# Kernel tuning notes

Measured on AMD Instinct MI355X. Metric: run time of the kernel, lower is better.

The kernel has to match this reference:

```python
import jax, jax.numpy as jnp
import numpy as np

B, T, I, H, O = 256, 512, 128, 256, 1


def setup_inputs() -> dict:
    key = jax.random.key(0)
    ks = jax.random.split(key, 7)
    s_ih = 1.0 / np.sqrt(H)
    return {
        "x": jax.random.normal(ks[0], (B, T, I), dtype=jnp.float32),
        "W_ih": jax.random.uniform(ks[1], (H, I), jnp.float32, -s_ih, s_ih),
        "W_hh": jax.random.uniform(ks[2], (H, H), jnp.float32, -s_ih, s_ih),
        "b_ih": jax.random.uniform(ks[3], (H,), jnp.float32, -s_ih, s_ih),
        "b_hh": jax.random.uniform(ks[4], (H,), jnp.float32, -s_ih, s_ih),
        "fc_w": jax.random.uniform(ks[5], (O, H), jnp.float32, -s_ih, s_ih),
        "fc_b": jax.random.uniform(ks[6], (O,), jnp.float32, -s_ih, s_ih),
    }


def reference(x, W_ih, W_hh, b_ih, b_hh, fc_w, fc_b):
    # Elman RNN (tanh), batch_first, single layer, h0 = zeros.
    # Only the last hidden state feeds the fc head, so scan carries h only.
    b = b_ih + b_hh
    xW = jnp.einsum('bti,hi->tbh', x, W_ih) + b  # precompute input projection [T,B,H]

    def step(h, xw_t):
        h = jnp.tanh(xw_t + h @ W_hh.T)
        return h, None

    h0 = jnp.zeros((x.shape[0], W_hh.shape[0]), dtype=x.dtype)
    h_last, _ = jax.lax.scan(step, h0, xW)
    return h_last @ fc_w.T + fc_b  # [B, O]
```

## Files before the change

### kernel.cpp

```cpp
#include <hip/hip_runtime.h>
#include <hip/hip_bf16.h>

#define B_ 256
#define T_ 512
#define I_ 128
#define H_ 256

#define SC 2.885390081777927f

typedef __bf16 bf16x8 __attribute__((ext_vector_type(8)));
typedef float  f32x4  __attribute__((ext_vector_type(4)));
typedef unsigned short u16;
typedef unsigned int   u32;

union U16x8Cast { uint4 v; bf16x8 b; };

__device__ inline u16 f2b(float f) {
    union { __bf16 h; u16 u; } c; c.h = (__bf16)f; return c.u;
}
__device__ inline bf16x8 pack8(float4 lo, float4 hi) {
    bf16x8 f;
    f[0]=(__bf16)lo.x; f[1]=(__bf16)lo.y; f[2]=(__bf16)lo.z; f[3]=(__bf16)lo.w;
    f[4]=(__bf16)hi.x; f[5]=(__bf16)hi.y; f[6]=(__bf16)hi.z; f[7]=(__bf16)hi.w;
    return f;
}
__device__ inline bf16x8 pack8s(float4 lo, float4 hi, float s) {
    bf16x8 f;
    f[0]=(__bf16)(lo.x*s); f[1]=(__bf16)(lo.y*s); f[2]=(__bf16)(lo.z*s); f[3]=(__bf16)(lo.w*s);
    f[4]=(__bf16)(hi.x*s); f[5]=(__bf16)(hi.y*s); f[6]=(__bf16)(hi.z*s); f[7]=(__bf16)(hi.w*s);
    return f;
}
__device__ inline uint2 pack4(float a, float b, float c, float d) {
    uint2 p;
    p.x = (u32)f2b(a) | ((u32)f2b(b) << 16);
    p.y = (u32)f2b(c) | ((u32)f2b(d) << 16);
    return p;
}
__device__ inline f32x4 b4_to_f32x4(uint2 u) {
    f32x4 r;
    r[0] = __uint_as_float(u.x << 16);
    r[1] = __uint_as_float(u.x & 0xFFFF0000u);
    r[2] = __uint_as_float(u.y << 16);
    r[3] = __uint_as_float(u.y & 0xFFFF0000u);
    return r;
}
__device__ inline float tanh_pre(float s) {
    float e = __builtin_amdgcn_exp2f(s);
    float r = __builtin_amdgcn_rcpf(1.f + e);
    return fmaf(-2.f, r, 1.f);
}

#define WG_BARRIER() asm volatile("s_waitcnt lgkmcnt(0)\n\ts_barrier" ::: "memory")

#define LDST 264
__global__ __launch_bounds__(256, 2) void xw_gemm_mfma(const float* __restrict__ x,
                                                       const float* __restrict__ W_ih,
                                                       const float* __restrict__ b_ih,
                                                       const float* __restrict__ b_hh,
                                                       u16* __restrict__ xw) {
    __shared__ u16 tile[64 * LDST];

    const int tid  = (int)threadIdx.x;
    const int wave = tid >> 6;
    const int lane = tid & 63;
    const int q    = lane >> 4;
    const int ml   = lane & 15;
    const int m0   = (int)blockIdx.x * 64;
    const int b    = m0 >> 9;
    const int t0   = m0 & 511;
    const int n0   = wave * 64;

    bf16x8 wA[4][4];
#pragma unroll
    for (int tau = 0; tau < 4; ++tau) {
        const float* wr = W_ih + (size_t)(n0 + tau * 16 + ml) * I_;
#pragma unroll
        for (int kap = 0; kap < 4; ++kap) {
            const int k0 = kap * 32 + q * 8;
            wA[tau][kap] = pack8s(*(const float4*)(wr + k0), *(const float4*)(wr + k0 + 4), SC);
        }
    }

    f32x4 acc[4][4];
#pragma unroll
    for (int mt = 0; mt < 4; ++mt)
#pragma unroll
        for (int tau = 0; tau < 4; ++tau) acc[mt][tau] = (f32x4)0.f;

#pragma unroll
    for (int kap = 0; kap < 4; ++kap) {
        bf16x8 xB[4];
#pragma unroll
        for (int mt = 0; mt < 4; ++mt) {
            const float* xr = x + (size_t)(m0 + mt * 16 + ml) * I_ + kap * 32 + q * 8;
            xB[mt] = pack8(*(const float4*)xr, *(const float4*)(xr + 4));
        }
#pragma unroll
        for (int mt = 0; mt < 4; ++mt)
#pragma unroll
            for (int tau = 0; tau < 4; ++tau)
                acc[mt][tau] = __builtin_amdgcn_mfma_f32_16x16x32_bf16(
                    wA[tau][kap], xB[mt], acc[mt][tau], 0, 0, 0);
    }

    float4 bias4[4];
#pragma unroll
    for (int tau = 0; tau < 4; ++tau) {
        const int n = n0 + tau * 16 + q * 4;
        float4 bi = *(const float4*)(b_ih + n);
        float4 bh = *(const float4*)(b_hh + n);
        bias4[tau] = make_float4((bi.x + bh.x) * SC, (bi.y + bh.y) * SC,
                                 (bi.z + bh.z) * SC, (bi.w + bh.w) * SC);
    }

#pragma unroll
    for (int mt = 0; mt < 4; ++mt) {
        const int row = mt * 16 + ml;
#pragma unroll
        for (int tau = 0; tau < 4; ++tau) {
            uint2 pk = pack4(acc[mt][tau][0] + bias4[tau].x,
                             acc[mt][tau][1] + bias4[tau].y,
                             acc[mt][tau][2] + bias4[tau].z,
                             acc[mt][tau][3] + bias4[tau].w);
            *(uint2*)(tile + row * LDST + n0 + tau * 16 + q * 4) = pk;
        }
    }
    __syncthreads();
#pragma unroll
    for (int s = 0; s < 4; ++s) {
        const int rr = s * 16 + (tid >> 4);
        const int c  = tid & 15;
        const uint4* srcp = (const uint4*)(tile + rr * LDST);
        uint4* dstp = (uint4*)(xw + ((size_t)(t0 + rr) * B_ + b) * H_);
        uint4 v0 = srcp[c];
        uint4 v1 = srcp[c + 16];
        dstp[c] = v0;
        dstp[c + 16] = v1;
    }
}

__global__ __launch_bounds__(512, 2) void rnn_scan_mfma(const u16* __restrict__ xw,
                                                        const float* __restrict__ W_hh,
                                                        const float* __restrict__ fc_w,
                                                        const float* __restrict__ fc_b,
                                                        float* __restrict__ out) {
    __shared__ __attribute__((aligned(16))) u16 hbuf[2][4096];
    __shared__ float red[8][16];

    const int tid  = (int)threadIdx.x;
    const int wave = tid >> 6;
    const int lane = tid & 63;
    const int q    = lane >> 4;
    const int m    = lane & 15;
    const int b0   = (int)blockIdx.x * 16;

    bf16x8 wf[2][8];
#pragma unroll
    for (int tau2 = 0; tau2 < 2; ++tau2) {
        const float* wr = W_hh + (size_t)(wave * 32 + tau2 * 16 + m) * H_;
#pragma unroll
        for (int kap = 0; kap < 8; ++kap) {
            const int k0 = kap * 32 + q * 8;
            wf[tau2][kap] = pack8s(*(const float4*)(wr + k0), *(const float4*)(wr + k0 + 4), SC);
        }
    }

    int widx[2];
#pragma unroll
    for (int tau2 = 0; tau2 < 2; ++tau2) {
        const int nbw = wave * 32 + tau2 * 16 + q * 4;
        widx[tau2] = (nbw >> 5) * 512 + (((nbw >> 3) & 3) * 16 + m) * 8 + (nbw & 7);
    }

    {
        uint4* p = (uint4*)&hbuf[0][0];
        const uint4 z = {0u, 0u, 0u, 0u};
        p[tid] = z;
    }
    WG_BARRIER();

    const u16* xwp = xw + (size_t)(b0 + m) * H_ + (wave * 32 + q * 4);
    const size_t tstride = (size_t)B_ * H_;

    uint2 pfA[2], pfB[2];
    pfA[0] = *(const uint2*)(xwp);
    pfA[1] = *(const uint2*)(xwp + 16);
    pfB[0] = *(const uint2*)(xwp + tstride);
    pfB[1] = *(const uint2*)(xwp + tstride + 16);

    int cur = 0;
    f32x4 acc[2];
    for (int tt = 0; tt < T_ / 2; ++tt) {
        {
            const int t = 2 * tt;
            acc[0] = b4_to_f32x4(pfA[0]);
            acc[1] = b4_to_f32x4(pfA[1]);
            if (t + 2 < T_) {
                const u16* pt = xwp + (size_t)(t + 2) * tstride;
                pfA[0] = *(const uint2*)(pt);
                pfA[1] = *(const uint2*)(pt + 16);
            }
            const uint4* hb = (const uint4*)&hbuf[cur][0];
#pragma unroll
            for (int kap = 0; kap < 8; ++kap) {
                U16x8Cast c; c.v = hb[kap * 64 + lane];
                acc[0] = __builtin_amdgcn_mfma_f32_16x16x32_bf16(wf[0][kap], c.b, acc[0], 0, 0, 0);
                acc[1] = __builtin_amdgcn_mfma_f32_16x16x32_bf16(wf[1][kap], c.b, acc[1], 0, 0, 0);
            }
            u16* wb = &hbuf[cur ^ 1][0];
#pragma unroll
            for (int tau2 = 0; tau2 < 2; ++tau2) {
                uint2 pk = pack4(tanh_pre(acc[tau2][0]), tanh_pre(acc[tau2][1]),
                                 tanh_pre(acc[tau2][2]), tanh_pre(acc[tau2][3]));
                *(uint2*)(wb + widx[tau2]) = pk;
            }
            WG_BARRIER();
            cur ^= 1;
        }
        {
            const int t = 2 * tt + 1;
            acc[0] = b4_to_f32x4(pfB[0]);
            acc[1] = b4_to_f32x4(pfB[1]);
            if (t + 2 < T_) {
                const u16* pt = xwp + (size_t)(t + 2) * tstride;
                pfB[0] = *(const uint2*)(pt);
                pfB[1] = *(const uint2*)(pt + 16);
            }
            const uint4* hb = (const uint4*)&hbuf[cur][0];
#pragma unroll
            for (int kap = 0; kap < 8; ++kap) {
                U16x8Cast c; c.v = hb[kap * 64 + lane];
                acc[0] = __builtin_amdgcn_mfma_f32_16x16x32_bf16(wf[0][kap], c.b, acc[0], 0, 0, 0);
                acc[1] = __builtin_amdgcn_mfma_f32_16x16x32_bf16(wf[1][kap], c.b, acc[1], 0, 0, 0);
            }
            if (t != T_ - 1) {
                u16* wb = &hbuf[cur ^ 1][0];
#pragma unroll
                for (int tau2 = 0; tau2 < 2; ++tau2) {
                    uint2 pk = pack4(tanh_pre(acc[tau2][0]), tanh_pre(acc[tau2][1]),
                                     tanh_pre(acc[tau2][2]), tanh_pre(acc[tau2][3]));
                    *(uint2*)(wb + widx[tau2]) = pk;
                }
                WG_BARRIER();
                cur ^= 1;
            }
        }
    }

    float4 fcw[2];
#pragma unroll
    for (int tau2 = 0; tau2 < 2; ++tau2)
        fcw[tau2] = *(const float4*)(fc_w + wave * 32 + tau2 * 16 + q * 4);

    float partial = 0.f;
#pragma unroll
    for (int tau2 = 0; tau2 < 2; ++tau2) {
        partial += tanh_pre(acc[tau2][0]) * fcw[tau2].x;
        partial += tanh_pre(acc[tau2][1]) * fcw[tau2].y;
        partial += tanh_pre(acc[tau2][2]) * fcw[tau2].z;
        partial += tanh_pre(acc[tau2][3]) * fcw[tau2].w;
    }
    partial += __shfl_xor(partial, 16);
    partial += __shfl_xor(partial, 32);
    __syncthreads();
    if (lane < 16) red[wave][m] = partial;
    __syncthreads();
    if (tid < 16) {
        float s = red[0][tid] + red[1][tid] + red[2][tid] + red[3][tid]
                + red[4][tid] + red[5][tid] + red[6][tid] + red[7][tid];
        out[b0 + tid] = s + fc_b[0];
    }
}

extern "C" void kernel_launch(void* const* d_in, const int* in_sizes, int n_in,
                              void* d_out, int out_size, void* d_ws, size_t ws_size,
                              hipStream_t stream) {
    const float* x    = (const float*)d_in[0];
    const float* W_ih = (const float*)d_in[1];
    const float* W_hh = (const float*)d_in[2];
    const float* b_ih = (const float*)d_in[3];
    const float* b_hh = (const float*)d_in[4];
    const float* fc_w = (const float*)d_in[5];
    const float* fc_b = (const float*)d_in[6];
    float* out = (float*)d_out;

    u16* xwbuf = (u16*)d_ws;
    xw_gemm_mfma<<<(B_ * T_) / 64, 256, 0, stream>>>(x, W_ih, b_ih, b_hh, xwbuf);
    rnn_scan_mfma<<<B_ / 16, 512, 0, stream>>>(xwbuf, W_hh, fc_w, fc_b, out);
}
```

Measured before the change: 387.1 us.

## Fuse input projection into recurrent scan kernel, dropping separate GEMM and workspace

Removes the separate xW GEMM kernel and its bf16 workspace round-trip. Each scan step now loads the raw x row for the next timestep and computes the input projection with extra MFMAs inside the recurrence, using W_ih fragments held in registers. This saves a kernel launch and the memory traffic for the intermediate, but it adds 8 MFMAs per step to the serial critical path, and only 16 blocks run, so HBM reads of x per step may add latency.

```diff
diff --git a/kernel.cpp b/kernel.cpp
--- a/kernel.cpp
+++ b/kernel.cpp
@@ -36,14 +36,6 @@
     p.y = (u32)f2b(c) | ((u32)f2b(d) << 16);
     return p;
 }
-__device__ inline f32x4 b4_to_f32x4(uint2 u) {
-    f32x4 r;
-    r[0] = __uint_as_float(u.x << 16);
-    r[1] = __uint_as_float(u.x & 0xFFFF0000u);
-    r[2] = __uint_as_float(u.y << 16);
-    r[3] = __uint_as_float(u.y & 0xFFFF0000u);
-    return r;
-}
 __device__ inline float tanh_pre(float s) {
     float e = __builtin_amdgcn_exp2f(s);
     float r = __builtin_amdgcn_rcpf(1.f + e);
@@ -52,98 +44,14 @@
 
 #define WG_BARRIER() asm volatile("s_waitcnt lgkmcnt(0)\n\ts_barrier" ::: "memory")
 
-#define LDST 264
-__global__ __launch_bounds__(256, 2) void xw_gemm_mfma(const float* __restrict__ x,
-                                                       const float* __restrict__ W_ih,
-                                                       const float* __restrict__ b_ih,
-                                                       const float* __restrict__ b_hh,
-                                                       u16* __restrict__ xw) {
-    __shared__ u16 tile[64 * LDST];
-
-    const int tid  = (int)threadIdx.x;
-    const int wave = tid >> 6;
-    const int lane = tid & 63;
-    const int q    = lane >> 4;
-    const int ml   = lane & 15;
-    const int m0   = (int)blockIdx.x * 64;
-    const int b    = m0 >> 9;
-    const int t0   = m0 & 511;
-    const int n0   = wave * 64;
-
-    bf16x8 wA[4][4];
-#pragma unroll
-    for (int tau = 0; tau < 4; ++tau) {
-        const float* wr = W_ih + (size_t)(n0 + tau * 16 + ml) * I_;
-#pragma unroll
-        for (int kap = 0; kap < 4; ++kap) {
-            const int k0 = kap * 32 + q * 8;
-            wA[tau][kap] = pack8s(*(const float4*)(wr + k0), *(const float4*)(wr + k0 + 4), SC);
-        }
-    }
-
-    f32x4 acc[4][4];
-#pragma unroll
-    for (int mt = 0; mt < 4; ++mt)
-#pragma unroll
-        for (int tau = 0; tau < 4; ++tau) acc[mt][tau] = (f32x4)0.f;
-
-#pragma unroll
-    for (int kap = 0; kap < 4; ++kap) {
-        bf16x8 xB[4];
-#pragma unroll
-        for (int mt = 0; mt < 4; ++mt) {
-            const float* xr = x + (size_t)(m0 + mt * 16 + ml) * I_ + kap * 32 + q * 8;
-            xB[mt] = pack8(*(const float4*)xr, *(const float4*)(xr + 4));
-        }
-#pragma unroll
-        for (int mt = 0; mt < 4; ++mt)
-#pragma unroll
-            for (int tau = 0; tau < 4; ++tau)
-                acc[mt][tau] = __builtin_amdgcn_mfma_f32_16x16x32_bf16(
-                    wA[tau][kap], xB[mt], acc[mt][tau], 0, 0, 0);
-    }
-
-    float4 bias4[4];
-#pragma unroll
-    for (int tau = 0; tau < 4; ++tau) {
-        const int n = n0 + tau * 16 + q * 4;
-        float4 bi = *(const float4*)(b_ih + n);
-        float4 bh = *(const float4*)(b_hh + n);
-        bias4[tau] = make_float4((bi.x + bh.x) * SC, (bi.y + bh.y) * SC,
-                                 (bi.z + bh.z) * SC, (bi.w + bh.w) * SC);
-    }
-
-#pragma unroll
-    for (int mt = 0; mt < 4; ++mt) {
-        const int row = mt * 16 + ml;
-#pragma unroll
-        for (int tau = 0; tau < 4; ++tau) {
-            uint2 pk = pack4(acc[mt][tau][0] + bias4[tau].x,
-                             acc[mt][tau][1] + bias4[tau].y,
-                             acc[mt][tau][2] + bias4[tau].z,
-                             acc[mt][tau][3] + bias4[tau].w);
-            *(uint2*)(tile + row * LDST + n0 + tau * 16 + q * 4) = pk;
-        }
-    }
-    __syncthreads();
-#pragma unroll
-    for (int s = 0; s < 4; ++s) {
-        const int rr = s * 16 + (tid >> 4);
-        const int c  = tid & 15;
-        const uint4* srcp = (const uint4*)(tile + rr * LDST);
-        uint4* dstp = (uint4*)(xw + ((size_t)(t0 + rr) * B_ + b) * H_);
-        uint4 v0 = srcp[c];
-        uint4 v1 = srcp[c + 16];
-        dstp[c] = v0;
-        dstp[c + 16] = v1;
-    }
-}
-
-__global__ __launch_bounds__(512, 2) void rnn_scan_mfma(const u16* __restrict__ xw,
-                                                        const float* __restrict__ W_hh,
-                                                        const float* __restrict__ fc_w,
-                                                        const float* __restrict__ fc_b,
-                                                        float* __restrict__ out) {
+__global__ __launch_bounds__(512, 1) void rnn_fused(const float* __restrict__ x,
+                                                    const float* __restrict__ W_ih,
+                                                    const float* __restrict__ W_hh,
+                                                    const float* __restrict__ b_ih,
+                                                    const float* __restrict__ b_hh,
+                                                    const float* __restrict__ fc_w,
+                                                    const float* __restrict__ fc_b,
+                                                    float* __restrict__ out) {
     __shared__ __attribute__((aligned(16))) u16 hbuf[2][4096];
     __shared__ float red[8][16];
 
@@ -164,6 +72,28 @@
             wf[tau2][kap] = pack8s(*(const float4*)(wr + k0), *(const float4*)(wr + k0 + 4), SC);
         }
     }
+    bf16x8 wi[2][4];
+#pragma unroll
+    for (int tau2 = 0; tau2 < 2; ++tau2) {
+        const float* wr = W_ih + (size_t)(wave * 32 + tau2 * 16 + m) * I_;
+#pragma unroll
+        for (int kap = 0; kap < 4; ++kap) {
+            const int k0 = kap * 32 + q * 8;
+            wi[tau2][kap] = pack8s(*(const float4*)(wr + k0), *(const float4*)(wr + k0 + 4), SC);
+        }
+    }
+
+    f32x4 bias2[2];
+#pragma unroll
+    for (int tau2 = 0; tau2 < 2; ++tau2) {
+        const int n = wave * 32 + tau2 * 16 + q * 4;
+        float4 bi = *(const float4*)(b_ih + n);
+        float4 bh = *(const float4*)(b_hh + n);
+        bias2[tau2][0] = (bi.x + bh.x) * SC;
+        bias2[tau2][1] = (bi.y + bh.y) * SC;
+        bias2[tau2][2] = (bi.z + bh.z) * SC;
+        bias2[tau2][3] = (bi.w + bh.w) * SC;
+    }
 
     int widx[2];
 #pragma unroll
@@ -177,36 +107,50 @@
         const uint4 z = {0u, 0u, 0u, 0u};
         p[tid] = z;
     }
-    WG_BARRIER();
-
-    const u16* xwp = xw + (size_t)(b0 + m) * H_ + (wave * 32 + q * 4);
-    const size_t tstride = (size_t)B_ * H_;
-
-    uint2 pfA[2], pfB[2];
-    pfA[0] = *(const uint2*)(xwp);
-    pfA[1] = *(const uint2*)(xwp + 16);
-    pfB[0] = *(const uint2*)(xwp + tstride);
-    pfB[1] = *(const uint2*)(xwp + tstride + 16);
+    __syncthreads();
+
+    const float* xrow = x + ((size_t)(b0 + m) * T_) * I_ + q * 8;
+    float4 xpf[8];
+#pragma unroll
+    for (int kap = 0; kap < 4; ++kap) {
+        xpf[2 * kap]     = *(const float4*)(xrow + kap * 32);
+        xpf[2 * kap + 1] = *(const float4*)(xrow + kap * 32 + 4);
+    }
 
     int cur = 0;
     f32x4 acc[2];
-    for (int tt = 0; tt < T_ / 2; ++tt) {
-        {
-            const int t = 2 * tt;
-            acc[0] = b4_to_f32x4(pfA[0]);
-            acc[1] = b4_to_f32x4(pfA[1]);
-            if (t + 2 < T_) {
-                const u16* pt = xwp + (size_t)(t + 2) * tstride;
-                pfA[0] = *(const uint2*)(pt);
-                pfA[1] = *(const uint2*)(pt + 16);
+    for (int t = 0; t < T_; ++t) {
+        const uint4* hb = (const uint4*)&hbuf[cur][0];
+        U16x8Cast cv[8];
+#pragma unroll
+        for (int kap = 0; kap < 8; ++kap) cv[kap].v = hb[kap * 64 + lane];
+
+        bf16x8 xB[4];
+#pragma unroll
+        for (int kap = 0; kap < 4; ++kap) xB[kap] = pack8(xpf[2 * kap], xpf[2 * kap + 1]);
+        acc[0] = bias2[0];
+        acc[1] = bias2[1];
+        if (t + 1 < T_) {
+            const float* xp = xrow + (size_t)(t + 1) * I_;
+#pragma unroll
+            for (int kap = 0; kap < 4; ++kap) {
+                xpf[2 * kap]     = *(const float4*)(xp + kap * 32);
+                xpf[2 * kap + 1] = *(const float4*)(xp + kap * 32 + 4);
             }
-            const uint4* hb = (const uint4*)&hbuf[cur][0];
-#pragma unroll
-            for (int kap = 0; kap < 8; ++kap) {
-                U16x8Cast c; c.v = hb[kap * 64 + lane];
-                acc[0] = __builtin_amdgcn_mfma_f32_16x16x32_bf16(wf[0][kap], c.b, acc[0], 0, 0, 0);
-                acc[1] = __builtin_amdgcn_mfma_f32_16x16x32_bf16(wf[1][kap], c.b, acc[1], 0, 0, 0);
-            }
+        }
+#pragma unroll
+        for (int kap = 0; kap < 4; ++kap) {
+            acc[0] = __builtin_amdgcn_mfma_f32_16x16x32_bf16(wi[0][kap], xB[kap], acc[0], 0, 0, 0);
+            acc[1] = __builtin_amdgcn_mfma_f32_16x16x32_bf16(wi[1][kap], xB[kap], acc[1], 0, 0, 0);
+        }
+
+#pragma unroll
+        for (int kap = 0; kap < 8; ++kap) {
+            acc[0] = __builtin_amdgcn_mfma_f32_16x16x32_bf16(wf[0][kap], cv[kap].b, acc[0], 0, 0, 0);
+            acc[1] = __builtin_amdgcn_mfma_f32_16x16x32_bf16(wf[1][kap], cv[kap].b, acc[1], 0, 0, 0);
+        }
+
+        if (t != T_ - 1) {
             u16* wb = &hbuf[cur ^ 1][0];
 #pragma unroll
             for (int tau2 = 0; tau2 < 2; ++tau2) {
@@ -216,34 +160,6 @@
             }
             WG_BARRIER();
             cur ^= 1;
-        }
-        {
-            const int t = 2 * tt + 1;
-            acc[0] = b4_to_f32x4(pfB[0]);
-            acc[1] = b4_to_f32x4(pfB[1]);
-            if (t + 2 < T_) {
-                const u16* pt = xwp + (size_t)(t + 2) * tstride;
-                pfB[0] = *(const uint2*)(pt);
-                pfB[1] = *(const uint2*)(pt + 16);
-            }
-            const uint4* hb = (const uint4*)&hbuf[cur][0];
-#pragma unroll
-            for (int kap = 0; kap < 8; ++kap) {
-                U16x8Cast c; c.v = hb[kap * 64 + lane];
-                acc[0] = __builtin_amdgcn_mfma_f32_16x16x32_bf16(wf[0][kap], c.b, acc[0], 0, 0, 0);
-                acc[1] = __builtin_amdgcn_mfma_f32_16x16x32_bf16(wf[1][kap], c.b, acc[1], 0, 0, 0);
-            }
-            if (t != T_ - 1) {
-                u16* wb = &hbuf[cur ^ 1][0];
-#pragma unroll
-                for (int tau2 = 0; tau2 < 2; ++tau2) {
-                    uint2 pk = pack4(tanh_pre(acc[tau2][0]), tanh_pre(acc[tau2][1]),
-                                     tanh_pre(acc[tau2][2]), tanh_pre(acc[tau2][3]));
-                    *(uint2*)(wb + widx[tau2]) = pk;
-                }
-                WG_BARRIER();
-                cur ^= 1;
-            }
         }
     }
 
@@ -284,7 +200,5 @@
     const float* fc_b = (const float*)d_in[6];
     float* out = (float*)d_out;
 
-    u16* xwbuf = (u16*)d_ws;
-    xw_gemm_mfma<<<(B_ * T_) / 64, 256, 0, stream>>>(x, W_ih, b_ih, b_hh, xwbuf);
-    rnn_scan_mfma<<<B_ / 16, 512, 0, stream>>>(xwbuf, W_hh, fc_w, fc_b, out);
-}
+    rnn_fused<<<B_ / 16, 512, 0, stream>>>(x, W_ih, W_hh, b_ih, b_hh, fc_w, fc_b, out);
+}
```

After: 1.179 ms. 3.05x slower.
